# Kernel optimization log

Measured on AMD Instinct MI355X. Metric: run time of the kernel, lower is better.

The kernel has to match this reference:

```python
import jax, jax.numpy as jnp
import numpy as np
import math

B, S, IN_DIM = 2048, 60, 211
D, H, L, DFF, NC = 192, 6, 3, 768, 35
DK = D // H


def make_pe(seq_len, d_model):
    pos = np.arange(seq_len)[:, None].astype(np.float32)
    div = np.exp(np.arange(0, d_model, 2).astype(np.float32) * (-math.log(10000.0) / d_model))
    pe = np.zeros((seq_len, d_model), dtype=np.float32)
    pe[:, 0::2] = np.sin(pos * div)
    pe[:, 1::2] = np.cos(pos * div)
    return jnp.asarray(pe)


def setup_inputs() -> dict:
    key = jax.random.key(0)
    ks = jax.random.split(key, 24)
    r = lambda k, shape, fan: jax.random.normal(k, shape, jnp.float32) * (1.0 / np.sqrt(fan))
    inp = {
        'x': jax.random.normal(ks[0], (B, S, IN_DIM), jnp.float32),
        'W_in': r(ks[1], (IN_DIM, D), IN_DIM), 'b_in': jnp.zeros((D,), jnp.float32),
        'pe': make_pe(S, D),
        'Wq': r(ks[2], (L, D, D), D), 'bq': jnp.zeros((L, D), jnp.float32),
        'Wk': r(ks[3], (L, D, D), D), 'bk': jnp.zeros((L, D), jnp.float32),
        'Wv': r(ks[4], (L, D, D), D), 'bv': jnp.zeros((L, D), jnp.float32),
        'Wo': r(ks[5], (L, D, D), D), 'bo': jnp.zeros((L, D), jnp.float32),
        'W1': r(ks[6], (L, D, DFF), D), 'b1': jnp.zeros((L, DFF), jnp.float32),
        'W2': r(ks[7], (L, DFF, D), DFF), 'b2': jnp.zeros((L, D), jnp.float32),
        'g1': jnp.ones((L, D), jnp.float32), 'be1': jnp.zeros((L, D), jnp.float32),
        'g2': jnp.ones((L, D), jnp.float32), 'be2': jnp.zeros((L, D), jnp.float32),
        'Wc1': r(ks[8], (D, D // 2), D), 'bc1': jnp.zeros((D // 2,), jnp.float32),
        'Wc2': r(ks[9], (D // 2, NC), D // 2), 'bc2': jnp.zeros((NC,), jnp.float32),
    }
    return inp


def layer_norm(x, g, b, eps=1e-5):
    mu = jnp.mean(x, axis=-1, keepdims=True)
    var = jnp.mean((x - mu) ** 2, axis=-1, keepdims=True)
    return (x - mu) * jax.lax.rsqrt(var + eps) * g + b


def mha(x, Wq, bq, Wk, bk, Wv, bv, Wo, bo):
    Bs, Ss, _ = x.shape
    q = (x @ Wq + bq).reshape(Bs, Ss, H, DK)
    k = (x @ Wk + bk).reshape(Bs, Ss, H, DK)
    v = (x @ Wv + bv).reshape(Bs, Ss, H, DK)
    scores = jnp.einsum('bqhd,bkhd->bhqk', q, k) / jnp.sqrt(jnp.float32(DK))
    attn = jax.nn.softmax(scores, axis=-1)
    ctx = jnp.einsum('bhqk,bkhd->bqhd', attn, v).reshape(Bs, Ss, D)
    return ctx @ Wo + bo


def encoder_layer(x, Wq, bq, Wk, bk, Wv, bv, Wo, bo, W1, b1, W2, b2, g1, be1, g2, be2):
    attn_out = mha(x, Wq, bq, Wk, bk, Wv, bv, Wo, bo)
    x = layer_norm(x + attn_out, g1, be1)
    ff = jax.nn.gelu(x @ W1 + b1, approximate=False) @ W2 + b2
    return layer_norm(x + ff, g2, be2)


def reference(x, W_in, b_in, pe, Wq, bq, Wk, bk, Wv, bv, Wo, bo,
              W1, b1, W2, b2, g1, be1, g2, be2, Wc1, bc1, Wc2, bc2):
    h = x @ W_in + b_in + pe  # [B,S,D]
    for l in range(L):
        h = encoder_layer(h, Wq[l], bq[l], Wk[l], bk[l], Wv[l], bv[l], Wo[l], bo[l],
                          W1[l], b1[l], W2[l], b2[l], g1[l], be1[l], g2[l], be2[l])
    hidden = jax.nn.gelu(h @ Wc1 + bc1, approximate=False)
    return hidden @ Wc2 + bc2  # [B,S,NC]
```

## Files before the change

kernel.cpp:

```cpp
#include <hip/hip_runtime.h>
#include <cmath>

#define B_   2048
#define S_   60
#define NTOK (B_*S_)
#define IND_ 211
#define D_   192
#define H_   6
#define DK_  32
#define L_   3
#define DFF_ 768
#define NC_  35
#define DH_  96

typedef unsigned short us_t;
typedef us_t us8 __attribute__((ext_vector_type(8)));
typedef us_t us4 __attribute__((ext_vector_type(4)));
typedef short sh8 __attribute__((ext_vector_type(8)));
typedef float f4 __attribute__((ext_vector_type(4)));

#define MFMA(a, b, cc) __builtin_amdgcn_mfma_f32_16x16x32_bf16((a), (b), (cc), 0, 0, 0)
#define ZACC(A, M, N) \
    for (int _i = 0; _i < (M); ++_i) \
        for (int _j = 0; _j < (N); ++_j) { \
            A[_i][_j][0] = 0.f; A[_i][_j][1] = 0.f; A[_i][_j][2] = 0.f; A[_i][_j][3] = 0.f; }
#define ZACC1(A, N) \
    for (int _j = 0; _j < (N); ++_j) { \
        A[_j][0] = 0.f; A[_j][1] = 0.f; A[_j][2] = 0.f; A[_j][3] = 0.f; }

__device__ __forceinline__ float bf2f(us_t u) {
    union { unsigned int i; float f; } v; v.i = ((unsigned int)u) << 16; return v.f;
}
__device__ __forceinline__ us_t f2bf(float f) {
    union { float f; unsigned int i; } v; v.f = f;
    unsigned int r = v.i + 0x7fffu + ((v.i >> 16) & 1u);
    return (us_t)(r >> 16);
}
__device__ __forceinline__ float gelu_f(float v) {
    float u = v * (0.7978845608f + 0.0356774081f * v * v);
    float e = __expf(2.f * u);
    float t = 1.f - 2.f / (e + 1.f);
    return 0.5f * v * (1.f + t);
}
__device__ __forceinline__ void gld16(const us_t* g, us_t* s) {
    __builtin_amdgcn_global_load_lds(
        (const __attribute__((address_space(1))) unsigned int*)(g),
        (__attribute__((address_space(3))) unsigned int*)(s), 16, 0, 0);
}

__global__ void prep_t(const float* __restrict__ in, us_t* __restrict__ out,
                       int K, int Kpad, int N)
{
    int e = blockIdx.x * 256 + threadIdx.x;
    if (e >= N * Kpad) return;
    int n = e / Kpad, kp = e % Kpad;
    out[e] = (kp < K) ? f2bf(in[(size_t)kp * N + n]) : (us_t)0;
}

__global__ void prep_ff(const float* __restrict__ W1, const float* __restrict__ W2,
                        us_t* __restrict__ WT)
{
    int e = blockIdx.x * 256 + threadIdx.x;
    if (e >= L_ * 48 * 8192) return;
    int l = e / (48 * 8192), r = e % (48 * 8192);
    int t = r / 8192, q = r % 8192;
    int col = q / 40, kk = q % 40;
    int s = t % 6, ph = (t / 6) & 1, cb = t / 12;
    us_t v = 0;
    if (kk < 32 && col < D_) {
        if (!ph) v = f2bf(W1[((size_t)l * D_ + s * 32 + kk) * DFF_ + cb * D_ + col]);
        else     v = f2bf(W2[((size_t)l * DFF_ + cb * D_ + s * 32 + kk) * D_ + col]);
    }
    WT[e] = v;
}

__global__ __launch_bounds__(256) void inp_mfma(
    const float* __restrict__ x, const us_t* __restrict__ Wint,
    const float* __restrict__ b_in, const float* __restrict__ pe,
    us_t* __restrict__ h)
{
    __shared__ __align__(16) char smem[29696 + 27648];
    us_t* Xs = (us_t*)smem;
    us_t* Ws = (us_t*)(smem + 29696);
    const int tid = threadIdx.x;
    const int lane = tid & 63, wid = tid >> 6;
    const int g = lane >> 4, c = lane & 15;
    const int wr = wid >> 1, wc = wid & 1;
    const int row0 = blockIdx.x * 64;

    for (int e = tid; e < 64 * 224; e += 256) {
        int tok = e / 224, kp = e % 224;
        float v = (kp < IND_) ? x[(size_t)(row0 + tok) * IND_ + kp] : 0.f;
        Xs[tok * 232 + kp] = f2bf(v);
    }

    f4 acc[2][6];
    ZACC(acc, 2, 6);
    for (int pc = 0; pc < 4; ++pc) {
        __syncthreads();
        const int nk = (pc < 3) ? 64 : 32;
        const int per = nk / 8;
        for (int e = tid; e < 192 * per; e += 256) {
            int rw = e / per, v = e % per;
            *(us8*)&Ws[rw * 72 + v * 8] =
                *(const us8*)&Wint[(size_t)rw * 224 + pc * 64 + v * 8];
        }
        __syncthreads();
        for (int kk = 0; kk < nk / 32; ++kk) {
            const int ka = pc * 64 + kk * 32 + g * 8;
            const int kw = kk * 32 + g * 8;
            sh8 a0 = *(const sh8*)&Xs[(32 * wr + c) * 232 + ka];
            sh8 a1 = *(const sh8*)&Xs[(32 * wr + 16 + c) * 232 + ka];
            #pragma unroll
            for (int ni = 0; ni < 6; ++ni) {
                sh8 bf = *(const sh8*)&Ws[(96 * wc + 16 * ni + c) * 72 + kw];
                acc[0][ni] = MFMA(a0, bf, acc[0][ni]);
                acc[1][ni] = MFMA(a1, bf, acc[1][ni]);
            }
        }
    }
    #pragma unroll
    for (int ni = 0; ni < 6; ++ni) {
        const int col = 96 * wc + 16 * ni + c;
        const float bv = b_in[col];
        #pragma unroll
        for (int mi = 0; mi < 2; ++mi)
            #pragma unroll
            for (int r = 0; r < 4; ++r) {
                int tokg = row0 + 32 * wr + 16 * mi + 4 * g + r;
                int s = tokg % S_;
                float val = acc[mi][ni][r] + bv + pe[(size_t)s * D_ + col];
                h[(size_t)tokg * D_ + col] = f2bf(val);
            }
    }
}

__global__ __launch_bounds__(512) void qkv_attn_wo(
    us_t* __restrict__ h,
    const us_t* __restrict__ Wqt, const us_t* __restrict__ Wkt,
    const us_t* __restrict__ Wvt, const us_t* __restrict__ Wot,
    const float* __restrict__ bq, const float* __restrict__ bk,
    const float* __restrict__ bv, const float* __restrict__ bo,
    const float* __restrict__ g1, const float* __restrict__ be1)
{
    __shared__ __align__(16) char smem[157696];
    us_t* Xs = (us_t*)smem;
    us_t* Qs = (us_t*)(smem + 25600);
    us_t* Ks = (us_t*)(smem + 51200);
    us_t* Vt = (us_t*)(smem + 76800);
    us_t* Ws = (us_t*)(smem + 104448);
    us_t* P0 = (us_t*)(smem + 104448);
    us_t* P1 = (us_t*)(smem + 113664);
    us_t* Cx = (us_t*)(smem + 132096);
    float* eL = (float*)(smem + 51200);

    const int tid = threadIdx.x;
    const int lane = tid & 63, wid = tid >> 6;
    const int g = lane >> 4, c = lane & 15;
    const int wr = wid >> 2, wc = wid & 3;
    us_t* hb = h + (size_t)blockIdx.x * (S_ * D_);

    for (int e = tid; e < 1536; e += 512) {
        int tok = e / 24, v = e % 24;
        us8 u = {0, 0, 0, 0, 0, 0, 0, 0};
        if (tok < S_) u = *(const us8*)&hb[(size_t)tok * D_ + v * 8];
        *(us8*)&Xs[tok * 200 + v * 8] = u;
    }

    for (int m = 0; m < 3; ++m) {
        const us_t* Wt = (m == 0) ? Wqt : (m == 1) ? Wkt : Wvt;
        const float* bb = (m == 0) ? bq : (m == 1) ? bk : bv;
        f4 acc[2][3];
        ZACC(acc, 2, 3);
        for (int pc = 0; pc < 3; ++pc) {
            __syncthreads();
            for (int e = tid; e < 1536; e += 512) {
                int rw = e >> 3, v = e & 7;
                *(us8*)&Ws[rw * 72 + v * 8] =
                    *(const us8*)&Wt[(size_t)rw * 192 + pc * 64 + v * 8];
            }
            __syncthreads();
            #pragma unroll
            for (int kk = 0; kk < 2; ++kk) {
                const int ka = pc * 64 + kk * 32 + g * 8;
                const int kw = kk * 32 + g * 8;
                sh8 a0 = *(const sh8*)&Xs[(32 * wr + c) * 200 + ka];
                sh8 a1 = *(const sh8*)&Xs[(32 * wr + 16 + c) * 200 + ka];
                #pragma unroll
                for (int ni = 0; ni < 3; ++ni) {
                    sh8 bf = *(const sh8*)&Ws[(48 * wc + 16 * ni + c) * 72 + kw];
                    acc[0][ni] = MFMA(a0, bf, acc[0][ni]);
                    acc[1][ni] = MFMA(a1, bf, acc[1][ni]);
                }
            }
        }
        #pragma unroll
        for (int ni = 0; ni < 3; ++ni) {
            const int col = 48 * wc + 16 * ni + c;
            const float bval = bb[col];
            #pragma unroll
            for (int mi = 0; mi < 2; ++mi)
                #pragma unroll
                for (int r = 0; r < 4; ++r) {
                    int tok = 32 * wr + 16 * mi + 4 * g + r;
                    us_t o = f2bf(acc[mi][ni][r] + bval);
                    if (m == 0)      Qs[tok * 200 + col] = o;
                    else if (m == 1) Ks[tok * 200 + col] = o;
                    else             Vt[col * 72 + tok] = o;
                }
        }
    }
    __syncthreads();

    const int hgrp = wid & 3;
    const int hsel = wid >> 2;
    for (int rr = 0; rr < 3; ++rr) {
        const int hh = 2 * rr + hsel;
        us_t* Pb = hsel ? P1 : P0;
        f4 sc[4];
        ZACC1(sc, 4);
        {
            const int ka = 32 * hh + g * 8;
            sh8 aq = *(const sh8*)&Qs[(16 * hgrp + c) * 200 + ka];
            #pragma unroll
            for (int ni = 0; ni < 4; ++ni) {
                sh8 bk8 = *(const sh8*)&Ks[(16 * ni + c) * 200 + ka];
                sc[ni] = MFMA(aq, bk8, sc[ni]);
            }
        }
        #pragma unroll
        for (int r = 0; r < 4; ++r) {
            float mx = -1e30f;
            #pragma unroll
            for (int ni = 0; ni < 4; ++ni) {
                float v = sc[ni][r] * 0.17677669529663687f;
                if (16 * ni + c >= S_) v = -1e30f;
                sc[ni][r] = v;
                mx = fmaxf(mx, v);
            }
            mx = fmaxf(mx, __shfl_xor(mx, 1));
            mx = fmaxf(mx, __shfl_xor(mx, 2));
            mx = fmaxf(mx, __shfl_xor(mx, 4));
            mx = fmaxf(mx, __shfl_xor(mx, 8));
            float sum = 0.f;
            #pragma unroll
            for (int ni = 0; ni < 4; ++ni) {
                float e = __expf(sc[ni][r] - mx);
                sc[ni][r] = e; sum += e;
            }
            sum += __shfl_xor(sum, 1);
            sum += __shfl_xor(sum, 2);
            sum += __shfl_xor(sum, 4);
            sum += __shfl_xor(sum, 8);
            const float inv = 1.f / sum;
            #pragma unroll
            for (int ni = 0; ni < 4; ++ni)
                Pb[(16 * hgrp + 4 * g + r) * 72 + 16 * ni + c] = f2bf(sc[ni][r] * inv);
        }
        __syncthreads();
        f4 ov[2];
        ZACC1(ov, 2);
        #pragma unroll
        for (int kk = 0; kk < 2; ++kk) {
            sh8 ap = *(const sh8*)&Pb[(16 * hgrp + c) * 72 + kk * 32 + g * 8];
            #pragma unroll
            for (int n2 = 0; n2 < 2; ++n2) {
                sh8 bv8 = *(const sh8*)&Vt[(32 * hh + 16 * n2 + c) * 72 + kk * 32 + g * 8];
                ov[n2] = MFMA(ap, bv8, ov[n2]);
            }
        }
        #pragma unroll
        for (int n2 = 0; n2 < 2; ++n2)
            #pragma unroll
            for (int r = 0; r < 4; ++r)
                Cx[(16 * hgrp + 4 * g + r) * 200 + 32 * hh + 16 * n2 + c] = f2bf(ov[n2][r]);
        __syncthreads();
    }

    f4 aw[2][3];
    ZACC(aw, 2, 3);
    for (int pc = 0; pc < 3; ++pc) {
        __syncthreads();
        for (int e = tid; e < 1536; e += 512) {
            int rw = e >> 3, v = e & 7;
            *(us8*)&Ws[rw * 72 + v * 8] =
                *(const us8*)&Wot[(size_t)rw * 192 + pc * 64 + v * 8];
        }
        __syncthreads();
        #pragma unroll
        for (int kk = 0; kk < 2; ++kk) {
            const int ka = pc * 64 + kk * 32 + g * 8;
            const int kw = kk * 32 + g * 8;
            sh8 a0 = *(const sh8*)&Cx[(32 * wr + c) * 200 + ka];
            sh8 a1 = *(const sh8*)&Cx[(32 * wr + 16 + c) * 200 + ka];
            #pragma unroll
            for (int ni = 0; ni < 3; ++ni) {
                sh8 bf = *(const sh8*)&Ws[(48 * wc + 16 * ni + c) * 72 + kw];
                aw[0][ni] = MFMA(a0, bf, aw[0][ni]);
                aw[1][ni] = MFMA(a1, bf, aw[1][ni]);
            }
        }
    }
    __syncthreads();
    #pragma unroll
    for (int ni = 0; ni < 3; ++ni) {
        const int col = 48 * wc + 16 * ni + c;
        const float bov = bo[col];
        #pragma unroll
        for (int mi = 0; mi < 2; ++mi)
            #pragma unroll
            for (int r = 0; r < 4; ++r) {
                int tok = 32 * wr + 16 * mi + 4 * g + r;
                eL[tok * 200 + col] = aw[mi][ni][r] + bov + bf2f(Xs[tok * 200 + col]);
            }
    }
    __syncthreads();
    {
        const int tok = tid >> 3, t8 = tid & 7;
        float vals[24], sum = 0.f, ssq = 0.f;
        #pragma unroll
        for (int jv = 0; jv < 6; ++jv) {
            float4 v4 = *(const float4*)&eL[tok * 200 + t8 * 24 + jv * 4];
            vals[jv*4+0] = v4.x; vals[jv*4+1] = v4.y; vals[jv*4+2] = v4.z; vals[jv*4+3] = v4.w;
            sum += v4.x + v4.y + v4.z + v4.w;
            ssq += v4.x*v4.x + v4.y*v4.y + v4.z*v4.z + v4.w*v4.w;
        }
        sum += __shfl_xor(sum, 1); sum += __shfl_xor(sum, 2); sum += __shfl_xor(sum, 4);
        ssq += __shfl_xor(ssq, 1); ssq += __shfl_xor(ssq, 2); ssq += __shfl_xor(ssq, 4);
        const float mean = sum * (1.f / D_);
        const float var  = ssq * (1.f / D_) - mean * mean;
        const float rstd = rsqrtf(var + 1e-5f);
        if (tok < S_) {
            #pragma unroll
            for (int jv = 0; jv < 6; ++jv) {
                us4 o4;
                #pragma unroll
                for (int j = 0; j < 4; ++j) {
                    int col = t8 * 24 + jv * 4 + j;
                    o4[j] = f2bf((vals[jv*4+j] - mean) * rstd * g1[col] + be1[col]);
                }
                *(us4*)&hb[(size_t)tok * D_ + t8 * 24 + jv * 4] = o4;
            }
        }
    }
}

__device__ __forceinline__ void ff_phase(const us_t* A, f4 (&acc)[2][6],
                                         const us_t* W, int s,
                                         int wr, int wc, int g, int c)
{
    const int ka = s * 32 + g * 8;
    sh8 a0 = *(const sh8*)&A[(32 * wr + c) * 200 + ka];
    sh8 a1 = *(const sh8*)&A[(32 * wr + 16 + c) * 200 + ka];
    #pragma unroll
    for (int ni = 0; ni < 6; ++ni) {
        sh8 bf = *(const sh8*)&W[(96 * wc + 16 * ni + c) * 40 + g * 8];
        acc[0][ni] = MFMA(a0, bf, acc[0][ni]);
        acc[1][ni] = MFMA(a1, bf, acc[1][ni]);
    }
}

__global__ __launch_bounds__(512) void ff_mfma(
    us_t* __restrict__ hio,
    const us_t* __restrict__ WT, const float* __restrict__ b1,
    const float* __restrict__ b2,
    const float* __restrict__ gamma, const float* __restrict__ beta)
{
    __shared__ __align__(16) char smem[151552];
    us_t* Xs  = (us_t*)smem;
    us_t* Ts  = (us_t*)(smem + 51200);
    us_t* Wsb = (us_t*)(smem + 102400);
    float* eL = (float*)(smem + 51200);

    const int tid = threadIdx.x;
    const int lane = tid & 63, wid = tid >> 6;
    const int g = lane >> 4, c = lane & 15;
    const int wr = wid >> 1, wc = wid & 1;
    const int row0 = blockIdx.x * 128;

    auto stage = [&](int t) {
        const us_t* src = WT + (size_t)t * 8192;
        us_t* dst = Wsb + (t % 3) * 8192;
        #pragma unroll
        for (int p = 0; p < 2; ++p) {
            const int i = wid + p * 8;
            gld16(src + i * 512 + lane * 8, dst + i * 512);
        }
    };

    for (int e = tid; e < 3072; e += 512) {
        int tok = e / 24, v = e % 24;
        *(us8*)&Xs[tok * 200 + v * 8] = *(const us8*)&hio[(size_t)(row0 + tok) * D_ + v * 8];
    }
    stage(0); stage(1);
    asm volatile("s_waitcnt vmcnt(2) lgkmcnt(0)" ::: "memory");
    __builtin_amdgcn_s_barrier();

    f4 acc1[2][6], acc2[2][6];
    ZACC(acc2, 2, 6);
    for (int t = 0; t < 48; ++t) {
        const int s = t % 6, ph = (t / 6) & 1;
        if (t <= 45) stage(t + 2);
        const us_t* W = Wsb + (t % 3) * 8192;
        if (!ph) {
            if (s == 0) ZACC(acc1, 2, 6);
            ff_phase(Xs, acc1, W, s, wr, wc, g, c);
            if (s == 5) {
                const int cb = t / 12;
                #pragma unroll
                for (int ni = 0; ni < 6; ++ni) {
                    const int col = 96 * wc + 16 * ni + c;
                    const float b1v = b1[cb * 192 + col];
                    #pragma unroll
                    for (int mi = 0; mi < 2; ++mi)
                        #pragma unroll
                        for (int r = 0; r < 4; ++r) {
                            int tok = 32 * wr + 16 * mi + 4 * g + r;
                            Ts[tok * 200 + col] = f2bf(gelu_f(acc1[mi][ni][r] + b1v));
                        }
                }
            }
        } else {
            ff_phase(Ts, acc2, W, s, wr, wc, g, c);
        }
        if (t <= 45) asm volatile("s_waitcnt vmcnt(2) lgkmcnt(0)" ::: "memory");
        else         asm volatile("s_waitcnt vmcnt(0) lgkmcnt(0)" ::: "memory");
        __builtin_amdgcn_s_barrier();
    }

    for (int p = 0; p < 2; ++p) {
        if (p) __syncthreads();
        if ((wr >> 1) == p) {
            #pragma unroll
            for (int ni = 0; ni < 6; ++ni) {
                const int col = 96 * wc + 16 * ni + c;
                const float b2v = b2[col];
                #pragma unroll
                for (int mi = 0; mi < 2; ++mi)
                    #pragma unroll
                    for (int r = 0; r < 4; ++r) {
                        int tok = 32 * wr + 16 * mi + 4 * g + r;
                        eL[(tok - 64 * p) * 200 + col] =
                            acc2[mi][ni][r] + b2v + bf2f(Xs[tok * 200 + col]);
                    }
            }
        }
        __syncthreads();
        {
            const int tl = tid >> 3, t8 = tid & 7;
            float vals[24], sum = 0.f, ssq = 0.f;
            #pragma unroll
            for (int jv = 0; jv < 6; ++jv) {
                float4 v4 = *(const float4*)&eL[tl * 200 + t8 * 24 + jv * 4];
                vals[jv*4+0] = v4.x; vals[jv*4+1] = v4.y;
                vals[jv*4+2] = v4.z; vals[jv*4+3] = v4.w;
                sum += v4.x + v4.y + v4.z + v4.w;
                ssq += v4.x*v4.x + v4.y*v4.y + v4.z*v4.z + v4.w*v4.w;
            }
            sum += __shfl_xor(sum, 1); sum += __shfl_xor(sum, 2); sum += __shfl_xor(sum, 4);
            ssq += __shfl_xor(ssq, 1); ssq += __shfl_xor(ssq, 2); ssq += __shfl_xor(ssq, 4);
            const float mean = sum * (1.f / D_);
            const float var  = ssq * (1.f / D_) - mean * mean;
            const float rstd = rsqrtf(var + 1e-5f);
            #pragma unroll
            for (int jv = 0; jv < 6; ++jv) {
                us4 o4;
                #pragma unroll
                for (int j = 0; j < 4; ++j) {
                    int col = t8 * 24 + jv * 4 + j;
                    o4[j] = f2bf((vals[jv*4+j] - mean) * rstd * gamma[col] + beta[col]);
                }
                *(us4*)&hio[(size_t)(row0 + 64 * p + tl) * D_ + t8 * 24 + jv * 4] = o4;
            }
        }
    }
}

__global__ __launch_bounds__(256) void clf1_mfma(
    const us_t* __restrict__ h, const us_t* __restrict__ Wc1t,
    const float* __restrict__ bc1, us_t* __restrict__ hid)
{
    __shared__ __align__(16) char smem[25600 + 13824];
    us_t* Xs = (us_t*)smem;
    us_t* Ws = (us_t*)(smem + 25600);
    const int tid = threadIdx.x;
    const int lane = tid & 63, wid = tid >> 6;
    const int g = lane >> 4, c = lane & 15;
    const int wr = wid >> 1, wc = wid & 1;
    const int row0 = blockIdx.x * 64;

    for (int e = tid; e < 1536; e += 256) {
        int tok = e / 24, v = e % 24;
        *(us8*)&Xs[tok * 200 + v * 8] = *(const us8*)&h[(size_t)(row0 + tok) * D_ + v * 8];
    }
    f4 acc[2][3];
    ZACC(acc, 2, 3);
    for (int pc = 0; pc < 3; ++pc) {
        __syncthreads();
        for (int e = tid; e < 768; e += 256) {
            int rw = e >> 3, v = e & 7;
            *(us8*)&Ws[rw * 72 + v * 8] =
                *(const us8*)&Wc1t[(size_t)rw * 192 + pc * 64 + v * 8];
        }
        __syncthreads();
        #pragma unroll
        for (int kk = 0; kk < 2; ++kk) {
            const int ka = pc * 64 + kk * 32 + g * 8;
            const int kw = kk * 32 + g * 8;
            sh8 a0 = *(const sh8*)&Xs[(32 * wr + c) * 200 + ka];
            sh8 a1 = *(const sh8*)&Xs[(32 * wr + 16 + c) * 200 + ka];
            #pragma unroll
            for (int ni = 0; ni < 3; ++ni) {
                sh8 bf = *(const sh8*)&Ws[(48 * wc + 16 * ni + c) * 72 + kw];
                acc[0][ni] = MFMA(a0, bf, acc[0][ni]);
                acc[1][ni] = MFMA(a1, bf, acc[1][ni]);
            }
        }
    }
    #pragma unroll
    for (int ni = 0; ni < 3; ++ni) {
        const int col = 48 * wc + 16 * ni + c;
        const float bv = bc1[col];
        #pragma unroll
        for (int mi = 0; mi < 2; ++mi)
            #pragma unroll
            for (int r = 0; r < 4; ++r) {
                int tok = row0 + 32 * wr + 16 * mi + 4 * g + r;
                hid[(size_t)tok * DH_ + col] = f2bf(gelu_f(acc[mi][ni][r] + bv));
            }
    }
}

__global__ __launch_bounds__(256) void clf2_kernel(
    const us_t* __restrict__ hid, const float* __restrict__ Wc2,
    const float* __restrict__ bc2, float* __restrict__ out)
{
    __shared__ us_t Hs[64 * 104];
    __shared__ float Wl[DH_ * NC_];
    __shared__ float bl[NC_];
    const int tid = threadIdx.x;
    const int row0 = blockIdx.x * 64;
    for (int e = tid; e < 768; e += 256) {
        int tok = e / 12, v = e % 12;
        *(us8*)&Hs[tok * 104 + v * 8] = *(const us8*)&hid[(size_t)(row0 + tok) * DH_ + v * 8];
    }
    for (int e = tid; e < DH_ * NC_; e += 256) Wl[e] = Wc2[e];
    if (tid < NC_) bl[tid] = bc2[tid];
    __syncthreads();
    for (int e = tid; e < 64 * NC_; e += 256) {
        const int tok = e / NC_, col = e % NC_;
        float acc = bl[col];
        #pragma unroll 8
        for (int kk = 0; kk < DH_; ++kk)
            acc = fmaf(bf2f(Hs[tok * 104 + kk]), Wl[kk * NC_ + col], acc);
        out[(size_t)(row0 + tok) * NC_ + col] = acc;
    }
}

extern "C" void kernel_launch(void* const* d_in, const int* in_sizes, int n_in,
                              void* d_out, int out_size, void* d_ws, size_t ws_size,
                              hipStream_t stream)
{
    const float* x    = (const float*)d_in[0];
    const float* W_in = (const float*)d_in[1];
    const float* b_in = (const float*)d_in[2];
    const float* pe   = (const float*)d_in[3];
    const float* Wq   = (const float*)d_in[4];
    const float* bq   = (const float*)d_in[5];
    const float* Wk   = (const float*)d_in[6];
    const float* bk   = (const float*)d_in[7];
    const float* Wv   = (const float*)d_in[8];
    const float* bv   = (const float*)d_in[9];
    const float* Wo   = (const float*)d_in[10];
    const float* bo   = (const float*)d_in[11];
    const float* W1   = (const float*)d_in[12];
    const float* b1   = (const float*)d_in[13];
    const float* W2   = (const float*)d_in[14];
    const float* b2   = (const float*)d_in[15];
    const float* g1   = (const float*)d_in[16];
    const float* be1  = (const float*)d_in[17];
    const float* g2   = (const float*)d_in[18];
    const float* be2  = (const float*)d_in[19];
    const float* Wc1  = (const float*)d_in[20];
    const float* bc1  = (const float*)d_in[21];
    const float* Wc2  = (const float*)d_in[22];
    const float* bc2  = (const float*)d_in[23];
    float* outp = (float*)d_out;

    us_t* h    = (us_t*)d_ws;
    us_t* hid  = h + (size_t)NTOK * D_;
    us_t* Wint = hid + (size_t)NTOK * DH_;
    us_t* Wqt  = Wint + 192 * 224;
    us_t* Wkt  = Wqt + 3 * 36864;
    us_t* Wvt  = Wkt + 3 * 36864;
    us_t* Wot  = Wvt + 3 * 36864;
    us_t* WT   = Wot + 3 * 36864;
    us_t* Wc1t = WT + (size_t)L_ * 48 * 8192;

    prep_t<<<168, 256, 0, stream>>>(W_in, Wint, IND_, 224, D_);
    for (int l = 0; l < L_; ++l) {
        prep_t<<<144, 256, 0, stream>>>(Wq + (size_t)l * 36864, Wqt + (size_t)l * 36864, 192, 192, 192);
        prep_t<<<144, 256, 0, stream>>>(Wk + (size_t)l * 36864, Wkt + (size_t)l * 36864, 192, 192, 192);
        prep_t<<<144, 256, 0, stream>>>(Wv + (size_t)l * 36864, Wvt + (size_t)l * 36864, 192, 192, 192);
        prep_t<<<144, 256, 0, stream>>>(Wo + (size_t)l * 36864, Wot + (size_t)l * 36864, 192, 192, 192);
    }
    prep_ff<<<(L_ * 48 * 8192 + 255) / 256, 256, 0, stream>>>(W1, W2, WT);
    prep_t<<<72, 256, 0, stream>>>(Wc1, Wc1t, 192, 192, DH_);

    inp_mfma<<<NTOK / 64, 256, 0, stream>>>(x, Wint, b_in, pe, h);

    for (int l = 0; l < L_; ++l) {
        qkv_attn_wo<<<B_, 512, 0, stream>>>(
            h,
            Wqt + (size_t)l * 36864, Wkt + (size_t)l * 36864,
            Wvt + (size_t)l * 36864, Wot + (size_t)l * 36864,
            bq + l * D_, bk + l * D_, bv + l * D_, bo + l * D_,
            g1 + l * D_, be1 + l * D_);
        ff_mfma<<<NTOK / 128, 512, 0, stream>>>(
            h, WT + (size_t)l * 48 * 8192, b1 + l * DFF_, b2 + l * D_,
            g2 + l * D_, be2 + l * D_);
    }

    clf1_mfma<<<NTOK / 64, 256, 0, stream>>>(h, Wc1t, bc1, hid);
    clf2_kernel<<<NTOK / 64, 256, 0, stream>>>(hid, Wc2, bc2, outp);
}
```

Baseline: 1.342 ms.

## Shrink FFN tile to 64 tokens with transposed MFMA and register LayerNorm

The FFN kernel now processes 64 tokens per block instead of 128 and swaps MFMA operands so weights are the A operand and activations the B operand. Each wave accumulates 6 tiles instead of 12. Weight staging drops the padded 40-element row stride to 32 and uses double instead of triple buffering, cutting shared memory from about 148KB to 75KB so more blocks can be resident. The final LayerNorm now runs from registers using shuffles plus a small cross-wave shared reduction instead of staging fp32 rows through LDS. The risks are that each weight tile loaded from global memory is reused across half as many tokens, unpadded LDS rows may cause bank conflicts, and the shallower prefetch plus a full barrier each step may expose load latency.

New measurement: 1.349 ms. Within noise of the previous version (+0.5%).

```diff
diff --git a/kernel.cpp b/kernel.cpp
--- a/kernel.cpp
+++ b/kernel.cpp
@@ -61,16 +61,14 @@
                         us_t* __restrict__ WT)
 {
     int e = blockIdx.x * 256 + threadIdx.x;
-    if (e >= L_ * 48 * 8192) return;
-    int l = e / (48 * 8192), r = e % (48 * 8192);
-    int t = r / 8192, q = r % 8192;
-    int col = q / 40, kk = q % 40;
-    int s = t % 6, ph = (t / 6) & 1, cb = t / 12;
-    us_t v = 0;
-    if (kk < 32 && col < D_) {
-        if (!ph) v = f2bf(W1[((size_t)l * D_ + s * 32 + kk) * DFF_ + cb * D_ + col]);
-        else     v = f2bf(W2[((size_t)l * DFF_ + cb * D_ + s * 32 + kk) * D_ + col]);
-    }
+    if (e >= L_ * 48 * 6144) return;
+    int l = e / (48 * 6144), r = e % (48 * 6144);
+    int t = r / 6144, q = r % 6144;
+    int col = q >> 5, kk = q & 31;
+    int cb = t / 12, ph = (t / 6) & 1, s = t % 6;
+    us_t v;
+    if (!ph) v = f2bf(W1[((size_t)l * D_ + s * 32 + kk) * DFF_ + cb * 192 + col]);
+    else     v = f2bf(W2[((size_t)l * DFF_ + cb * 192 + s * 32 + kk) * D_ + col]);
     WT[e] = v;
 }
 
@@ -345,134 +343,107 @@
     }
 }
 
-__device__ __forceinline__ void ff_phase(const us_t* A, f4 (&acc)[2][6],
-                                         const us_t* W, int s,
-                                         int wr, int wc, int g, int c)
-{
-    const int ka = s * 32 + g * 8;
-    sh8 a0 = *(const sh8*)&A[(32 * wr + c) * 200 + ka];
-    sh8 a1 = *(const sh8*)&A[(32 * wr + 16 + c) * 200 + ka];
-    #pragma unroll
-    for (int ni = 0; ni < 6; ++ni) {
-        sh8 bf = *(const sh8*)&W[(96 * wc + 16 * ni + c) * 40 + g * 8];
-        acc[0][ni] = MFMA(a0, bf, acc[0][ni]);
-        acc[1][ni] = MFMA(a1, bf, acc[1][ni]);
-    }
-}
-
 __global__ __launch_bounds__(512) void ff_mfma(
     us_t* __restrict__ hio,
     const us_t* __restrict__ WT, const float* __restrict__ b1,
     const float* __restrict__ b2,
     const float* __restrict__ gamma, const float* __restrict__ beta)
 {
-    __shared__ __align__(16) char smem[151552];
+    __shared__ __align__(16) char smem[76800];
     us_t* Xs  = (us_t*)smem;
-    us_t* Ts  = (us_t*)(smem + 51200);
-    us_t* Wsb = (us_t*)(smem + 102400);
-    float* eL = (float*)(smem + 51200);
+    us_t* Ts  = (us_t*)(smem + 25600);
+    us_t* Wsb = (us_t*)(smem + 51200);
+    float* Sm = (float*)(smem + 75776);
 
     const int tid = threadIdx.x;
     const int lane = tid & 63, wid = tid >> 6;
     const int g = lane >> 4, c = lane & 15;
-    const int wr = wid >> 1, wc = wid & 1;
-    const int row0 = blockIdx.x * 128;
+    const int wr = wid >> 1;
+    const int wc = wid & 1;
+    const int row0 = blockIdx.x * 64;
 
     auto stage = [&](int t) {
-        const us_t* src = WT + (size_t)t * 8192;
-        us_t* dst = Wsb + (t % 3) * 8192;
-        #pragma unroll
-        for (int p = 0; p < 2; ++p) {
-            const int i = wid + p * 8;
+        const us_t* src = WT + (size_t)t * 6144;
+        us_t* dst = Wsb + (t & 1) * 6144;
+        for (int i = wid; i < 12; i += 8)
             gld16(src + i * 512 + lane * 8, dst + i * 512);
-        }
     };
 
-    for (int e = tid; e < 3072; e += 512) {
+    for (int e = tid; e < 1536; e += 512) {
         int tok = e / 24, v = e % 24;
         *(us8*)&Xs[tok * 200 + v * 8] = *(const us8*)&hio[(size_t)(row0 + tok) * D_ + v * 8];
     }
-    stage(0); stage(1);
-    asm volatile("s_waitcnt vmcnt(2) lgkmcnt(0)" ::: "memory");
-    __builtin_amdgcn_s_barrier();
-
-    f4 acc1[2][6], acc2[2][6];
-    ZACC(acc2, 2, 6);
+    stage(0);
+    __syncthreads();
+
+    f4 acc1[6], acc2[6];
+    ZACC1(acc2, 6);
     for (int t = 0; t < 48; ++t) {
-        const int s = t % 6, ph = (t / 6) & 1;
-        if (t <= 45) stage(t + 2);
-        const us_t* W = Wsb + (t % 3) * 8192;
+        const int s = t % 6, ph = (t / 6) & 1, cb = t / 12;
+        if (t < 47) stage(t + 1);
+        const us_t* W = Wsb + (t & 1) * 6144;
         if (!ph) {
-            if (s == 0) ZACC(acc1, 2, 6);
-            ff_phase(Xs, acc1, W, s, wr, wc, g, c);
+            if (s == 0) ZACC1(acc1, 6);
+            sh8 xb = *(const sh8*)&Xs[(16 * wr + c) * 200 + s * 32 + g * 8];
+            #pragma unroll
+            for (int ni = 0; ni < 6; ++ni) {
+                sh8 wa = *(const sh8*)&W[(96 * wc + 16 * ni + c) * 32 + g * 8];
+                acc1[ni] = MFMA(wa, xb, acc1[ni]);
+            }
             if (s == 5) {
-                const int cb = t / 12;
                 #pragma unroll
                 for (int ni = 0; ni < 6; ++ni) {
-                    const int col = 96 * wc + 16 * ni + c;
-                    const float b1v = b1[cb * 192 + col];
+                    const int d0 = 96 * wc + 16 * ni + 4 * g;
+                    us4 o4;
                     #pragma unroll
-                    for (int mi = 0; mi < 2; ++mi)
-                        #pragma unroll
-                        for (int r = 0; r < 4; ++r) {
-                            int tok = 32 * wr + 16 * mi + 4 * g + r;
-                            Ts[tok * 200 + col] = f2bf(gelu_f(acc1[mi][ni][r] + b1v));
-                        }
+                    for (int r = 0; r < 4; ++r)
+                        o4[r] = f2bf(gelu_f(acc1[ni][r] + b1[cb * 192 + d0 + r]));
+                    *(us4*)&Ts[(16 * wr + c) * 200 + d0] = o4;
                 }
             }
         } else {
-            ff_phase(Ts, acc2, W, s, wr, wc, g, c);
-        }
-        if (t <= 45) asm volatile("s_waitcnt vmcnt(2) lgkmcnt(0)" ::: "memory");
-        else         asm volatile("s_waitcnt vmcnt(0) lgkmcnt(0)" ::: "memory");
-        __builtin_amdgcn_s_barrier();
-    }
-
-    for (int p = 0; p < 2; ++p) {
-        if (p) __syncthreads();
-        if ((wr >> 1) == p) {
+            sh8 tb = *(const sh8*)&Ts[(16 * wr + c) * 200 + s * 32 + g * 8];
             #pragma unroll
             for (int ni = 0; ni < 6; ++ni) {
-                const int col = 96 * wc + 16 * ni + c;
-                const float b2v = b2[col];
-                #pragma unroll
-                for (int mi = 0; mi < 2; ++mi)
-                    #pragma unroll
-                    for (int r = 0; r < 4; ++r) {
-                        int tok = 32 * wr + 16 * mi + 4 * g + r;
-                        eL[(tok - 64 * p) * 200 + col] =
-                            acc2[mi][ni][r] + b2v + bf2f(Xs[tok * 200 + col]);
-                    }
-            }
-        }
-        __syncthreads();
-        {
-            const int tl = tid >> 3, t8 = tid & 7;
-            float vals[24], sum = 0.f, ssq = 0.f;
-            #pragma unroll
-            for (int jv = 0; jv < 6; ++jv) {
-                float4 v4 = *(const float4*)&eL[tl * 200 + t8 * 24 + jv * 4];
-                vals[jv*4+0] = v4.x; vals[jv*4+1] = v4.y;
-                vals[jv*4+2] = v4.z; vals[jv*4+3] = v4.w;
-                sum += v4.x + v4.y + v4.z + v4.w;
-                ssq += v4.x*v4.x + v4.y*v4.y + v4.z*v4.z + v4.w*v4.w;
-            }
-            sum += __shfl_xor(sum, 1); sum += __shfl_xor(sum, 2); sum += __shfl_xor(sum, 4);
-            ssq += __shfl_xor(ssq, 1); ssq += __shfl_xor(ssq, 2); ssq += __shfl_xor(ssq, 4);
-            const float mean = sum * (1.f / D_);
-            const float var  = ssq * (1.f / D_) - mean * mean;
-            const float rstd = rsqrtf(var + 1e-5f);
-            #pragma unroll
-            for (int jv = 0; jv < 6; ++jv) {
-                us4 o4;
-                #pragma unroll
-                for (int j = 0; j < 4; ++j) {
-                    int col = t8 * 24 + jv * 4 + j;
-                    o4[j] = f2bf((vals[jv*4+j] - mean) * rstd * gamma[col] + beta[col]);
-                }
-                *(us4*)&hio[(size_t)(row0 + 64 * p + tl) * D_ + t8 * 24 + jv * 4] = o4;
-            }
-        }
+                sh8 wa = *(const sh8*)&W[(96 * wc + 16 * ni + c) * 32 + g * 8];
+                acc2[ni] = MFMA(wa, tb, acc2[ni]);
+            }
+        }
+        __syncthreads();
+    }
+
+    float v[6][4];
+    float sum = 0.f, ssq = 0.f;
+    const int xrow = (16 * wr + c) * 200;
+    #pragma unroll
+    for (int ni = 0; ni < 6; ++ni)
+        #pragma unroll
+        for (int r = 0; r < 4; ++r) {
+            const int dcol = 96 * wc + 16 * ni + 4 * g + r;
+            float val = acc2[ni][r] + b2[dcol] + bf2f(Xs[xrow + dcol]);
+            v[ni][r] = val; sum += val; ssq += val * val;
+        }
+    sum += __shfl_xor(sum, 16); sum += __shfl_xor(sum, 32);
+    ssq += __shfl_xor(ssq, 16); ssq += __shfl_xor(ssq, 32);
+    if (g == 0) {
+        Sm[((0 * 2 + wc) * 4 + wr) * 16 + c] = sum;
+        Sm[((1 * 2 + wc) * 4 + wr) * 16 + c] = ssq;
+    }
+    __syncthreads();
+    sum += Sm[((0 * 2 + (1 - wc)) * 4 + wr) * 16 + c];
+    ssq += Sm[((1 * 2 + (1 - wc)) * 4 + wr) * 16 + c];
+    const float mean = sum * (1.f / D_);
+    const float var  = ssq * (1.f / D_) - mean * mean;
+    const float rstd = rsqrtf(var + 1e-5f);
+    us_t* orow = hio + (size_t)(row0 + 16 * wr + c) * D_;
+    #pragma unroll
+    for (int ni = 0; ni < 6; ++ni) {
+        const int d0 = 96 * wc + 16 * ni + 4 * g;
+        us4 o4;
+        #pragma unroll
+        for (int r = 0; r < 4; ++r)
+            o4[r] = f2bf((v[ni][r] - mean) * rstd * gamma[d0 + r] + beta[d0 + r]);
+        *(us4*)&orow[d0] = o4;
     }
 }
 
@@ -595,7 +566,7 @@
     us_t* Wvt  = Wkt + 3 * 36864;
     us_t* Wot  = Wvt + 3 * 36864;
     us_t* WT   = Wot + 3 * 36864;
-    us_t* Wc1t = WT + (size_t)L_ * 48 * 8192;
+    us_t* Wc1t = WT + (size_t)L_ * 48 * 6144;
 
     prep_t<<<168, 256, 0, stream>>>(W_in, Wint, IND_, 224, D_);
     for (int l = 0; l < L_; ++l) {
@@ -604,7 +575,7 @@
         prep_t<<<144, 256, 0, stream>>>(Wv + (size_t)l * 36864, Wvt + (size_t)l * 36864, 192, 192, 192);
         prep_t<<<144, 256, 0, stream>>>(Wo + (size_t)l * 36864, Wot + (size_t)l * 36864, 192, 192, 192);
     }
-    prep_ff<<<(L_ * 48 * 8192 + 255) / 256, 256, 0, stream>>>(W1, W2, WT);
+    prep_ff<<<(L_ * 48 * 6144 + 255) / 256, 256, 0, stream>>>(W1, W2, WT);
     prep_t<<<72, 256, 0, stream>>>(Wc1, Wc1t, 192, 192, DH_);
 
     inp_mfma<<<NTOK / 64, 256, 0, stream>>>(x, Wint, b_in, pe, h);
@@ -616,8 +587,8 @@
             Wvt + (size_t)l * 36864, Wot + (size_t)l * 36864,
             bq + l * D_, bk + l * D_, bv + l * D_, bo + l * D_,
             g1 + l * D_, be1 + l * D_);
-        ff_mfma<<<NTOK / 128, 512, 0, stream>>>(
-            h, WT + (size_t)l * 48 * 8192, b1 + l * DFF_, b2 + l * D_,
+        ff_mfma<<<NTOK / 64, 512, 0, stream>>>(
+            h, WT + (size_t)l * 48 * 6144, b1 + l * DFF_, b2 + l * D_,
             g2 + l * D_, be2 + l * D_);
     }
 
```
